# Optimization experiments

Measured on AMD Instinct MI355X. Metric: run time of the kernel, lower is better.

## Reference

```python
import jax, jax.numpy as jnp
import numpy as np

N = 50000
E = 640000
R = 8


def setup_inputs() -> dict:
    key = jax.random.key(0)
    ks = jax.random.split(key, 12)
    in_c, hid_c, out_c = 128, 128, 64
    s1 = 1.0 / np.sqrt(in_c)
    s2 = 1.0 / np.sqrt(hid_c)
    s3 = 1.0 / np.sqrt(out_c)
    return {
        "x": jax.random.normal(ks[0], (N, in_c), dtype=jnp.float32),
        "edge_index": jax.random.randint(ks[1], (2, E), 0, N),
        "edge_type": jax.random.randint(ks[2], (E,), 0, R),
        # layer 1: per-relation weights, root weight, bias
        "W1": jax.random.uniform(ks[3], (R, in_c, hid_c), minval=-s1, maxval=s1, dtype=jnp.float32),
        "root1": jax.random.uniform(ks[4], (in_c, hid_c), minval=-s1, maxval=s1, dtype=jnp.float32),
        "b1": jnp.zeros((hid_c,), dtype=jnp.float32),
        # layer 2
        "W2": jax.random.uniform(ks[5], (R, hid_c, out_c), minval=-s2, maxval=s2, dtype=jnp.float32),
        "root2": jax.random.uniform(ks[6], (hid_c, out_c), minval=-s2, maxval=s2, dtype=jnp.float32),
        "b2": jnp.zeros((out_c,), dtype=jnp.float32),
        # classifier
        "Wc": jax.random.uniform(ks[7], (out_c, 2), minval=-s3, maxval=s3, dtype=jnp.float32),
        "bc": jnp.zeros((2,), dtype=jnp.float32),
    }


def _rgcn_layer(x, edge_index, edge_type, W, root, b):
    # PyG RGCNConv with aggr='mean': per relation r, mean-aggregate source
    # features over edges of type r into destinations, then apply W_r.
    # out = sum_r mean_agg_r(x) @ W_r + x @ root + b
    src, dst = edge_index[0], edge_index[1]
    msgs = x[src]  # [E, Fin] gather
    seg = edge_type * N + dst  # combined (relation, dst) segment id
    sums = jax.ops.segment_sum(msgs, seg, num_segments=R * N)  # [R*N, Fin]
    cnt = jax.ops.segment_sum(jnp.ones((msgs.shape[0],), x.dtype), seg, num_segments=R * N)
    mean = sums / jnp.maximum(cnt, 1.0)[:, None]  # zero-degree -> 0
    mean = mean.reshape(R, N, x.shape[1])  # [R, N, Fin]
    out = jnp.einsum("rnf,rfo->no", mean, W) + x @ root + b
    return out


def reference(x, edge_index, edge_type, W1, root1, b1, W2, root2, b2, Wc, bc):
    h = jax.nn.relu(_rgcn_layer(x, edge_index, edge_type, W1, root1, b1))
    # dropout (p=0.3) is identity in eval mode
    h = jax.nn.relu(_rgcn_layer(h, edge_index, edge_type, W2, root2, b2))
    logits = h @ Wc + bc  # [N, 2]
    return logits
```

## Files before the change

kernel.cpp:

```cpp
#include <hip/hip_runtime.h>

#define NN 50000
#define EE 640000
#define RR 8
#define CAP 64

typedef __bf16 bf16x8 __attribute__((ext_vector_type(8)));
typedef float  f32x4  __attribute__((ext_vector_type(4)));
typedef const __attribute__((address_space(1))) unsigned int* gas_p;
typedef __attribute__((address_space(3))) unsigned int* las_p;

__device__ __forceinline__ unsigned short f2b(float f) {
  unsigned int u = __float_as_uint(f);
  u += 0x7fffu + ((u >> 16) & 1u);
  return (unsigned short)(u >> 16);
}
__device__ __forceinline__ float b2f(unsigned short h) {
  return __uint_as_float(((unsigned int)h) << 16);
}

__device__ __forceinline__ float edge_scale(unsigned int e, int lane, int deg) {
  unsigned long long valid = __ballot(lane < deg);
  unsigned long long m0 = __ballot((e >> 16) & 1u);
  unsigned long long m1 = __ballot((e >> 17) & 1u);
  unsigned long long m2 = __ballot((e >> 18) & 1u);
  unsigned long long mm = ((e >> 16) & 1u ? m0 : ~m0);
  mm &= ((e >> 17) & 1u ? m1 : ~m1);
  mm &= ((e >> 18) & 1u ? m2 : ~m2);
  mm &= valid;
  return (lane < deg) ? __builtin_amdgcn_rcpf((float)__popcll(mm)) : 0.f;
}

#define CONV_N 1600000
#define B1_N (1152 * 128)
#define B2_N (640 * 128)
__global__ void k_prologue(const float* __restrict__ x, unsigned short* __restrict__ xb,
                           const float* __restrict__ W1, const float* __restrict__ root1,
                           unsigned short* __restrict__ B1T,
                           const float* __restrict__ W2, const float* __restrict__ root2,
                           unsigned short* __restrict__ B2T,
                           int* __restrict__ cursor) {
  int t = blockIdx.x * 256 + threadIdx.x;
  if (t < CONV_N) {
    float4 v = reinterpret_cast<const float4*>(x)[t];
    ushort4 o = make_ushort4(f2b(v.x), f2b(v.y), f2b(v.z), f2b(v.w));
    reinterpret_cast<ushort4*>(xb)[t] = o;
    return;
  }
  t -= CONV_N;
  if (t < B1_N) {
    int j = t >> 7, k = t & 127;
    float v = (j < 1024) ? W1[((j >> 7) << 14) + (k << 7) + (j & 127)]
                         : root1[(k << 7) + (j - 1024)];
    B1T[t] = f2b(v);
    return;
  }
  t -= B1_N;
  if (t < B2_N) {
    int j = t >> 7, k = t & 127;
    float v = 0.0f;
    if (j < 512)      v = W2[((j >> 6) << 13) + (k << 6) + (j & 63)];
    else if (j < 576) v = root2[(k << 6) + (j - 512)];
    B2T[t] = f2b(v);
    return;
  }
  t -= B2_N;
  if (t < NN) cursor[t] = 0;
}

template <bool EDGES>
__global__ __launch_bounds__(256, 3) void k_gemm(
    const unsigned short* __restrict__ A, const unsigned short* __restrict__ BT,
    unsigned short* __restrict__ Y, float* __restrict__ rootOut,
    const float* __restrict__ bias, int M, int nsplit, int nroot, int nsub,
    const int* __restrict__ srcI, const int* __restrict__ dstI,
    const int* __restrict__ typ, int* __restrict__ cursor,
    unsigned int* __restrict__ entries) {
  __shared__ __align__(16) unsigned short Bs[2][64 * 128];
  const int tid = threadIdx.x;

  if (EDGES && blockIdx.y == 0) {
    const int stride = gridDim.x * 256;
    for (int e = blockIdx.x * 256 + tid; e < EE; e += stride) {
      int d = dstI[e], r = typ[e];
      int pos = atomicAdd(&cursor[d], 1);
      if (pos < CAP)
        entries[d * CAP + pos] = (unsigned int)srcI[e] | ((unsigned int)r << 16);
    }
    return;
  }

  const int m0 = blockIdx.x * 128;
  const int cg = EDGES ? (blockIdx.y - 1) : blockIdx.y;
  const int n0g = cg * nsub * 64;
  const int lane = tid & 63;
  const int wave = tid >> 6;
  const int wm = (wave >> 1) << 6;
  const int wn = (wave & 1) << 5;
  const int l15 = lane & 15;
  const int quad = lane >> 4;

  {
    const unsigned short* Gb = BT + (size_t)n0g * 128;
#pragma unroll
    for (int c = 0; c < 4; ++c) {
      int L = tid + c * 256;
      int r = L >> 4, c16 = L & 15;
      int j = c16 ^ (r & 15);
      __builtin_amdgcn_global_load_lds(
          (gas_p)(const void*)(Gb + (size_t)r * 128 + j * 8),
          (las_p)(void*)(Bs[0] + r * 128 + c16 * 8), 16, 0, 0);
    }
  }

  bf16x8 af[4][4];
#pragma unroll
  for (int kk = 0; kk < 4; ++kk)
#pragma unroll
    for (int i = 0; i < 4; ++i)
      af[kk][i] = *reinterpret_cast<const bf16x8*>(
          A + (size_t)(m0 + wm + i * 16 + l15) * 128 + (kk * 4 + quad) * 8);

  __syncthreads();

  const int tr = lane >> 2;
  const int tc = lane & 3;
  const int sl0 = ((tc & 1) << 1) * 16 + tr;
  const int sl1 = sl0 + 16;
  const bool thi = (tc & 2) != 0;

  int buf = 0;
  for (int s = 0; s < nsub; ++s) {
    if (s + 1 < nsub) {
      const unsigned short* Gb = BT + (size_t)(n0g + (s + 1) * 64) * 128;
      unsigned short* Lb = Bs[buf ^ 1];
#pragma unroll
      for (int c = 0; c < 4; ++c) {
        int L = tid + c * 256;
        int r = L >> 4, c16 = L & 15;
        int j = c16 ^ (r & 15);
        __builtin_amdgcn_global_load_lds(
            (gas_p)(const void*)(Gb + (size_t)r * 128 + j * 8),
            (las_p)(void*)(Lb + r * 128 + c16 * 8), 16, 0, 0);
      }
    }

    f32x4 acc[4][2] = {};
    const unsigned short* Bc = Bs[buf];
#pragma unroll
    for (int kk = 0; kk < 4; ++kk) {
      const int sw = ((kk * 4 + quad) ^ l15) * 8;
      bf16x8 bfr[2];
#pragma unroll
      for (int j = 0; j < 2; ++j)
        bfr[j] = *reinterpret_cast<const bf16x8*>(&Bc[(wn + j * 16 + l15) * 128 + sw]);
#pragma unroll
      for (int i = 0; i < 4; ++i)
#pragma unroll
        for (int j = 0; j < 2; ++j)
          acc[i][j] = __builtin_amdgcn_mfma_f32_16x16x32_bf16(bfr[j], af[kk][i], acc[i][j], 0, 0, 0);
    }
    __syncthreads();

    const int scol = n0g + s * 64;
    if (scol >= nsplit) {
#pragma unroll
      for (int i = 0; i < 4; ++i) {
        const int m = wm + i * 16 + l15;
        if (m0 + m >= M) continue;
#pragma unroll
        for (int j = 0; j < 2; ++j) {
          const int col = scol + wn + j * 16 + quad * 4 - nsplit;
          if (col < nroot) {
            float4 b4 = *reinterpret_cast<const float4*>(&bias[col]);
            float4 v = make_float4(acc[i][j][0] + b4.x, acc[i][j][1] + b4.y,
                                   acc[i][j][2] + b4.z, acc[i][j][3] + b4.w);
            *reinterpret_cast<float4*>(&rootOut[(size_t)(m0 + m) * nroot + col]) = v;
          }
        }
      }
    } else {
#pragma unroll
      for (int i = 0; i < 4; ++i) {
        uint2 pk0, pk1;
        pk0.x = (unsigned int)f2b(acc[i][0][0]) | ((unsigned int)f2b(acc[i][0][1]) << 16);
        pk0.y = (unsigned int)f2b(acc[i][0][2]) | ((unsigned int)f2b(acc[i][0][3]) << 16);
        pk1.x = (unsigned int)f2b(acc[i][1][0]) | ((unsigned int)f2b(acc[i][1][1]) << 16);
        pk1.y = (unsigned int)f2b(acc[i][1][2]) | ((unsigned int)f2b(acc[i][1][3]) << 16);
        unsigned int a0x = __shfl(pk0.x, sl0, 64), a0y = __shfl(pk0.y, sl0, 64);
        unsigned int a1x = __shfl(pk1.x, sl0, 64), a1y = __shfl(pk1.y, sl0, 64);
        unsigned int b0x = __shfl(pk0.x, sl1, 64), b0y = __shfl(pk0.y, sl1, 64);
        unsigned int b1x = __shfl(pk1.x, sl1, 64), b1y = __shfl(pk1.y, sl1, 64);
        uint4 o;
        o.x = thi ? a1x : a0x;
        o.y = thi ? a1y : a0y;
        o.z = thi ? b1x : b0x;
        o.w = thi ? b1y : b0y;
        const int m = wm + i * 16 + tr;
        if (m0 + m < M)
          *reinterpret_cast<uint4*>(&Y[(size_t)(m0 + m) * nsplit + scol + wn + tc * 8]) = o;
      }
    }
    buf ^= 1;
  }
}

#define ACC8(pk, s)                                          \
  a[0] += b2f((unsigned short)pk.x) * s;                     \
  a[1] += __uint_as_float(pk.x & 0xffff0000u) * s;           \
  a[2] += b2f((unsigned short)pk.y) * s;                     \
  a[3] += __uint_as_float(pk.y & 0xffff0000u) * s;           \
  a[4] += b2f((unsigned short)pk.z) * s;                     \
  a[5] += __uint_as_float(pk.z & 0xffff0000u) * s;           \
  a[6] += b2f((unsigned short)pk.w) * s;                     \
  a[7] += __uint_as_float(pk.w & 0xffff0000u) * s;

__global__ void k_agg1(const unsigned int* __restrict__ entries,
                       const int* __restrict__ cursor,
                       const unsigned short* __restrict__ y,
                       const float* __restrict__ hpre,
                       unsigned int* __restrict__ hbf) {
  const int d = blockIdx.x * 4 + (threadIdx.x >> 6);
  const int lane = threadIdx.x & 63;
  int deg = cursor[d];
  if (deg > CAP) deg = CAP;
  unsigned int e = (lane < deg) ? entries[d * CAP + lane] : 0u;
  float sc = edge_scale(e, lane, deg);

  const int g = lane >> 4;
  const int l16 = lane & 15;

  float4 h0, h1;
  if (g == 0) {
    const float4* hp = reinterpret_cast<const float4*>(hpre) + (size_t)d * 32 + l16 * 2;
    h0 = hp[0];
    h1 = hp[1];
  }

  float a[8] = {};
  const int T = (deg + 15) >> 4;
  for (int t = 0; t < T; ++t) {
    const int base = t * 16 + g;
    unsigned int e0 = __shfl(e, base, 64);       float s0 = __shfl(sc, base, 64);
    unsigned int e1 = __shfl(e, base + 4, 64);   float s1 = __shfl(sc, base + 4, 64);
    unsigned int e2 = __shfl(e, base + 8, 64);   float s2 = __shfl(sc, base + 8, 64);
    unsigned int e3 = __shfl(e, base + 12, 64);  float s3 = __shfl(sc, base + 12, 64);
    uint4 p0 = *reinterpret_cast<const uint4*>(
        y + (((size_t)(e0 & 0xffffu)) << 10) + (((e0 >> 16) & 7u) << 7) + (l16 << 3));
    uint4 p1 = *reinterpret_cast<const uint4*>(
        y + (((size_t)(e1 & 0xffffu)) << 10) + (((e1 >> 16) & 7u) << 7) + (l16 << 3));
    uint4 p2 = *reinterpret_cast<const uint4*>(
        y + (((size_t)(e2 & 0xffffu)) << 10) + (((e2 >> 16) & 7u) << 7) + (l16 << 3));
    uint4 p3 = *reinterpret_cast<const uint4*>(
        y + (((size_t)(e3 & 0xffffu)) << 10) + (((e3 >> 16) & 7u) << 7) + (l16 << 3));
    ACC8(p0, s0);
    ACC8(p1, s1);
    ACC8(p2, s2);
    ACC8(p3, s3);
  }
#pragma unroll
  for (int j = 0; j < 8; ++j) {
    a[j] += __shfl_xor(a[j], 16, 64);
    a[j] += __shfl_xor(a[j], 32, 64);
  }
  if (g == 0) {
    float v0 = fmaxf(a[0] + h0.x, 0.f), v1 = fmaxf(a[1] + h0.y, 0.f);
    float v2 = fmaxf(a[2] + h0.z, 0.f), v3 = fmaxf(a[3] + h0.w, 0.f);
    float v4 = fmaxf(a[4] + h1.x, 0.f), v5 = fmaxf(a[5] + h1.y, 0.f);
    float v6 = fmaxf(a[6] + h1.z, 0.f), v7 = fmaxf(a[7] + h1.w, 0.f);
    uint4 o;
    o.x = (unsigned int)f2b(v0) | ((unsigned int)f2b(v1) << 16);
    o.y = (unsigned int)f2b(v2) | ((unsigned int)f2b(v3) << 16);
    o.z = (unsigned int)f2b(v4) | ((unsigned int)f2b(v5) << 16);
    o.w = (unsigned int)f2b(v6) | ((unsigned int)f2b(v7) << 16);
    reinterpret_cast<uint4*>(hbf)[(size_t)d * 16 + l16] = o;
  }
}

__global__ void k_agg2(const unsigned int* __restrict__ entries,
                       const int* __restrict__ cursor,
                       const unsigned short* __restrict__ y,
                       const float* __restrict__ hpre,
                       const float* __restrict__ Wc, const float* __restrict__ bc,
                       float* __restrict__ out) {
  const int d = blockIdx.x * 4 + (threadIdx.x >> 6);
  const int lane = threadIdx.x & 63;
  int deg = cursor[d];
  if (deg > CAP) deg = CAP;
  unsigned int e = (lane < deg) ? entries[d * CAP + lane] : 0u;
  float sc = edge_scale(e, lane, deg);

  const int g = lane >> 3;
  const int l8 = lane & 7;

  const float4* hp = reinterpret_cast<const float4*>(hpre) + (size_t)d * 16 + l8 * 2;
  float4 h0 = hp[0];
  float4 h1 = hp[1];

  float a[8] = {};
  const int T = (deg + 31) >> 5;
  for (int t = 0; t < T; ++t) {
    const int base = t * 32 + g;
    unsigned int e0 = __shfl(e, base, 64);       float s0 = __shfl(sc, base, 64);
    unsigned int e1 = __shfl(e, base + 8, 64);   float s1 = __shfl(sc, base + 8, 64);
    unsigned int e2 = __shfl(e, base + 16, 64);  float s2 = __shfl(sc, base + 16, 64);
    unsigned int e3 = __shfl(e, base + 24, 64);  float s3 = __shfl(sc, base + 24, 64);
    uint4 p0 = *reinterpret_cast<const uint4*>(
        y + (((size_t)(e0 & 0xffffu)) << 9) + (((e0 >> 16) & 7u) << 6) + (l8 << 3));
    uint4 p1 = *reinterpret_cast<const uint4*>(
        y + (((size_t)(e1 & 0xffffu)) << 9) + (((e1 >> 16) & 7u) << 6) + (l8 << 3));
    uint4 p2 = *reinterpret_cast<const uint4*>(
        y + (((size_t)(e2 & 0xffffu)) << 9) + (((e2 >> 16) & 7u) << 6) + (l8 << 3));
    uint4 p3 = *reinterpret_cast<const uint4*>(
        y + (((size_t)(e3 & 0xffffu)) << 9) + (((e3 >> 16) & 7u) << 6) + (l8 << 3));
    ACC8(p0, s0);
    ACC8(p1, s1);
    ACC8(p2, s2);
    ACC8(p3, s3);
  }
#pragma unroll
  for (int j = 0; j < 8; ++j) {
    a[j] += __shfl_xor(a[j], 8, 64);
    a[j] += __shfl_xor(a[j], 16, 64);
    a[j] += __shfl_xor(a[j], 32, 64);
  }
  float v0 = fmaxf(a[0] + h0.x, 0.f), v1 = fmaxf(a[1] + h0.y, 0.f);
  float v2 = fmaxf(a[2] + h0.z, 0.f), v3 = fmaxf(a[3] + h0.w, 0.f);
  float v4 = fmaxf(a[4] + h1.x, 0.f), v5 = fmaxf(a[5] + h1.y, 0.f);
  float v6 = fmaxf(a[6] + h1.z, 0.f), v7 = fmaxf(a[7] + h1.w, 0.f);
  const float4* wc4 = reinterpret_cast<const float4*>(Wc) + l8 * 4;
  float4 w0 = wc4[0], w1 = wc4[1], w2 = wc4[2], w3 = wc4[3];
  float p0 = v0 * w0.x + v1 * w0.z + v2 * w1.x + v3 * w1.z
           + v4 * w2.x + v5 * w2.z + v6 * w3.x + v7 * w3.z;
  float p1 = v0 * w0.y + v1 * w0.w + v2 * w1.y + v3 * w1.w
           + v4 * w2.y + v5 * w2.w + v6 * w3.y + v7 * w3.w;
  p0 += __shfl_xor(p0, 1, 64); p1 += __shfl_xor(p1, 1, 64);
  p0 += __shfl_xor(p0, 2, 64); p1 += __shfl_xor(p1, 2, 64);
  p0 += __shfl_xor(p0, 4, 64); p1 += __shfl_xor(p1, 4, 64);
  if (lane == 0) {
    out[d * 2 + 0] = p0 + bc[0];
    out[d * 2 + 1] = p1 + bc[1];
  }
}

extern "C" void kernel_launch(void* const* d_in, const int* in_sizes, int n_in,
                              void* d_out, int out_size, void* d_ws, size_t ws_size,
                              hipStream_t stream) {
  const float* x     = (const float*)d_in[0];
  const int*   ei    = (const int*)d_in[1];
  const int*   et    = (const int*)d_in[2];
  const float* W1    = (const float*)d_in[3];
  const float* root1 = (const float*)d_in[4];
  const float* b1    = (const float*)d_in[5];
  const float* W2    = (const float*)d_in[6];
  const float* root2 = (const float*)d_in[7];
  const float* b2    = (const float*)d_in[8];
  const float* Wc    = (const float*)d_in[9];
  const float* bc    = (const float*)d_in[10];
  const int* srcI = ei;
  const int* dstI = ei + EE;

  char* ws = (char*)d_ws;
  unsigned short* xb      = (unsigned short*)(ws);
  unsigned int*   hbf     = (unsigned int*)(ws);
  unsigned short* B1T     = (unsigned short*)(ws + 12800000);
  unsigned short* B2T     = (unsigned short*)(ws + 13094912);
  int*            cursor  = (int*)(ws + 13258752);
  unsigned int*   entries = (unsigned int*)(ws + 13458752);
  float*          hpre    = (float*)(ws + 26258752);
  unsigned short* y1      = (unsigned short*)(ws + 51858752);
  unsigned short* y2      = y1;

  const int PRO_N = CONV_N + B1_N + B2_N + NN;
  k_prologue<<<(PRO_N + 255) / 256, 256, 0, stream>>>(x, xb, W1, root1, B1T,
                                                      W2, root2, B2T, cursor);

  k_gemm<true><<<dim3(391, 4), 256, 0, stream>>>(xb, B1T, y1, hpre, b1, NN, 1024, 128, 6,
                                                 srcI, dstI, et, cursor, entries);
  k_agg1<<<NN / 4, 256, 0, stream>>>(entries, cursor, y1, hpre, hbf);

  k_gemm<false><<<dim3(391, 2), 256, 0, stream>>>((const unsigned short*)hbf, B2T, y2, hpre, b2,
                                                  NN, 512, 64, 5,
                                                  nullptr, nullptr, nullptr, nullptr, nullptr);
  k_agg2<<<NN / 4, 256, 0, stream>>>(entries, cursor, y2, hpre, Wc, bc, (float*)d_out);
}
```

Before: 259.9 us.

## Move edge bucketing from GEMM kernel into prologue and zero cursors via memset

Edge bucketing (the atomic cursor increments and entry writes) moves out of the first GEMM's extra grid row into the elementwise prologue, one thread per edge. Cursor zeroing becomes a hipMemsetAsync before the prologue. The GEMM drops its template and edge arguments and declares a higher launch-bounds occupancy hint. This gives the GEMM a uniform grid, but the edge pass no longer overlaps with GEMM work and there is one extra memset launch.

```diff
diff --git a/kernel.cpp b/kernel.cpp
--- a/kernel.cpp
+++ b/kernel.cpp
@@ -39,7 +39,9 @@
                            unsigned short* __restrict__ B1T,
                            const float* __restrict__ W2, const float* __restrict__ root2,
                            unsigned short* __restrict__ B2T,
-                           int* __restrict__ cursor) {
+                           const int* __restrict__ srcI, const int* __restrict__ dstI,
+                           const int* __restrict__ typ,
+                           int* __restrict__ cursor, unsigned int* __restrict__ entries) {
   int t = blockIdx.x * 256 + threadIdx.x;
   if (t < CONV_N) {
     float4 v = reinterpret_cast<const float4*>(x)[t];
@@ -65,34 +67,22 @@
     return;
   }
   t -= B2_N;
-  if (t < NN) cursor[t] = 0;
-}
-
-template <bool EDGES>
-__global__ __launch_bounds__(256, 3) void k_gemm(
+  if (t < EE) {
+    int d = dstI[t], r = typ[t];
+    int pos = atomicAdd(&cursor[d], 1);
+    if (pos < CAP)
+      entries[d * CAP + pos] = (unsigned int)srcI[t] | ((unsigned int)r << 16);
+  }
+}
+
+__global__ __launch_bounds__(256, 4) void k_gemm(
     const unsigned short* __restrict__ A, const unsigned short* __restrict__ BT,
     unsigned short* __restrict__ Y, float* __restrict__ rootOut,
-    const float* __restrict__ bias, int M, int nsplit, int nroot, int nsub,
-    const int* __restrict__ srcI, const int* __restrict__ dstI,
-    const int* __restrict__ typ, int* __restrict__ cursor,
-    unsigned int* __restrict__ entries) {
+    const float* __restrict__ bias, int M, int nsplit, int nroot, int nsub) {
   __shared__ __align__(16) unsigned short Bs[2][64 * 128];
   const int tid = threadIdx.x;
-
-  if (EDGES && blockIdx.y == 0) {
-    const int stride = gridDim.x * 256;
-    for (int e = blockIdx.x * 256 + tid; e < EE; e += stride) {
-      int d = dstI[e], r = typ[e];
-      int pos = atomicAdd(&cursor[d], 1);
-      if (pos < CAP)
-        entries[d * CAP + pos] = (unsigned int)srcI[e] | ((unsigned int)r << 16);
-    }
-    return;
-  }
-
   const int m0 = blockIdx.x * 128;
-  const int cg = EDGES ? (blockIdx.y - 1) : blockIdx.y;
-  const int n0g = cg * nsub * 64;
+  const int n0g = blockIdx.y * nsub * 64;
   const int lane = tid & 63;
   const int wave = tid >> 6;
   const int wm = (wave >> 1) << 6;
@@ -371,16 +361,17 @@
   unsigned short* y1      = (unsigned short*)(ws + 51858752);
   unsigned short* y2      = y1;
 
-  const int PRO_N = CONV_N + B1_N + B2_N + NN;
+  hipMemsetAsync(cursor, 0, 200000, stream);
+
+  const int PRO_N = CONV_N + B1_N + B2_N + EE;
   k_prologue<<<(PRO_N + 255) / 256, 256, 0, stream>>>(x, xb, W1, root1, B1T,
-                                                      W2, root2, B2T, cursor);
-
-  k_gemm<true><<<dim3(391, 4), 256, 0, stream>>>(xb, B1T, y1, hpre, b1, NN, 1024, 128, 6,
-                                                 srcI, dstI, et, cursor, entries);
+                                                      W2, root2, B2T,
+                                                      srcI, dstI, et, cursor, entries);
+
+  k_gemm<<<dim3(391, 3), 256, 0, stream>>>(xb, B1T, y1, hpre, b1, NN, 1024, 128, 6);
   k_agg1<<<NN / 4, 256, 0, stream>>>(entries, cursor, y1, hpre, hbf);
 
-  k_gemm<false><<<dim3(391, 2), 256, 0, stream>>>((const unsigned short*)hbf, B2T, y2, hpre, b2,
-                                                  NN, 512, 64, 5,
-                                                  nullptr, nullptr, nullptr, nullptr, nullptr);
+  k_gemm<<<dim3(391, 2), 256, 0, stream>>>((const unsigned short*)hbf, B2T, y2, hpre, b2,
+                                           NN, 512, 64, 5);
   k_agg2<<<NN / 4, 256, 0, stream>>>(entries, cursor, y2, hpre, Wc, bc, (float*)d_out);
 }
```

Result: slower. 300.2 us (+15.5%).

## Interleave edge-bucketing blocks with GEMM blocks in a flat 1D grid

Applied to the files above, without the earlier changes.

Layer 1's edge bucketing used to run as a y=0 grid row of grid-stride blocks. It is now spread across 2500 one-edge-per-thread blocks, interleaved two-to-one with the 1173 GEMM tile blocks in a flat 1D grid. The aim is for the atomic-heavy scatter work to overlap with GEMM tiles across CUs rather than sitting in a few long blocks. Cursor zeroing moves from the prologue kernel to a hipMemsetAsync, which adds a separate stream operation. The second GEMM is also flattened to 1D with the same tile mapping.

```diff
diff --git a/kernel.cpp b/kernel.cpp
--- a/kernel.cpp
+++ b/kernel.cpp
@@ -38,8 +38,7 @@
                            const float* __restrict__ W1, const float* __restrict__ root1,
                            unsigned short* __restrict__ B1T,
                            const float* __restrict__ W2, const float* __restrict__ root2,
-                           unsigned short* __restrict__ B2T,
-                           int* __restrict__ cursor) {
+                           unsigned short* __restrict__ B2T) {
   int t = blockIdx.x * 256 + threadIdx.x;
   if (t < CONV_N) {
     float4 v = reinterpret_cast<const float4*>(x)[t];
@@ -62,11 +61,12 @@
     if (j < 512)      v = W2[((j >> 6) << 13) + (k << 6) + (j & 63)];
     else if (j < 576) v = root2[(k << 6) + (j - 512)];
     B2T[t] = f2b(v);
-    return;
-  }
-  t -= B2_N;
-  if (t < NN) cursor[t] = 0;
-}
+  }
+}
+
+#define NBG1 1173
+#define NBE  2500
+#define FSPLIT (3 * NBG1)
 
 template <bool EDGES>
 __global__ __launch_bounds__(256, 3) void k_gemm(
@@ -79,20 +79,32 @@
   __shared__ __align__(16) unsigned short Bs[2][64 * 128];
   const int tid = threadIdx.x;
 
-  if (EDGES && blockIdx.y == 0) {
-    const int stride = gridDim.x * 256;
-    for (int e = blockIdx.x * 256 + tid; e < EE; e += stride) {
-      int d = dstI[e], r = typ[e];
-      int pos = atomicAdd(&cursor[d], 1);
-      if (pos < CAP)
-        entries[d * CAP + pos] = (unsigned int)srcI[e] | ((unsigned int)r << 16);
-    }
-    return;
-  }
-
-  const int m0 = blockIdx.x * 128;
-  const int cg = EDGES ? (blockIdx.y - 1) : blockIdx.y;
-  const int n0g = cg * nsub * 64;
+  int bg;
+  if (EDGES) {
+    const int bid = blockIdx.x;
+    int be = -1;
+    if (bid < FSPLIT) {
+      if (bid % 3 == 0) bg = bid / 3;
+      else              be = 2 * (bid / 3) + (bid % 3) - 1;
+    } else {
+      be = 2 * NBG1 + (bid - FSPLIT);
+    }
+    if (be >= 0) {
+      int e = be * 256 + tid;
+      if (e < EE) {
+        int d = dstI[e], r = typ[e];
+        int pos = atomicAdd(&cursor[d], 1);
+        if (pos < CAP)
+          entries[d * CAP + pos] = (unsigned int)srcI[e] | ((unsigned int)r << 16);
+      }
+      return;
+    }
+  } else {
+    bg = blockIdx.x;
+  }
+
+  const int m0 = (bg % 391) * 128;
+  const int n0g = (bg / 391) * nsub * 64;
   const int lane = tid & 63;
   const int wave = tid >> 6;
   const int wm = (wave >> 1) << 6;
@@ -371,16 +383,19 @@
   unsigned short* y1      = (unsigned short*)(ws + 51858752);
   unsigned short* y2      = y1;
 
-  const int PRO_N = CONV_N + B1_N + B2_N + NN;
+  hipMemsetAsync(cursor, 0, 200000, stream);
+
+  const int PRO_N = CONV_N + B1_N + B2_N;
   k_prologue<<<(PRO_N + 255) / 256, 256, 0, stream>>>(x, xb, W1, root1, B1T,
-                                                      W2, root2, B2T, cursor);
-
-  k_gemm<true><<<dim3(391, 4), 256, 0, stream>>>(xb, B1T, y1, hpre, b1, NN, 1024, 128, 6,
-                                                 srcI, dstI, et, cursor, entries);
+                                                      W2, root2, B2T);
+
+  k_gemm<true><<<dim3(NBG1 + NBE), 256, 0, stream>>>(xb, B1T, y1, hpre, b1,
+                                                     NN, 1024, 128, 6,
+                                                     srcI, dstI, et, cursor, entries);
   k_agg1<<<NN / 4, 256, 0, stream>>>(entries, cursor, y1, hpre, hbf);
 
-  k_gemm<false><<<dim3(391, 2), 256, 0, stream>>>((const unsigned short*)hbf, B2T, y2, hpre, b2,
-                                                  NN, 512, 64, 5,
-                                                  nullptr, nullptr, nullptr, nullptr, nullptr);
+  k_gemm<false><<<dim3(391 * 2), 256, 0, stream>>>((const unsigned short*)hbf, B2T, y2, hpre, b2,
+                                                   NN, 512, 64, 5,
+                                                   nullptr, nullptr, nullptr, nullptr, nullptr);
   k_agg2<<<NN / 4, 256, 0, stream>>>(entries, cursor, y2, hpre, Wc, bc, (float*)d_out);
 }
```

New measurement: 247.0 us. 1.05x faster.
